# Performance work log

Measured on AMD Instinct MI355X. Metric: run time of the kernel, lower is better.

Reference implementation:

```python
import jax, jax.numpy as jnp
import numpy as np

B, N, C_S, C_Z, C, H, PQ, PV = 1, 512, 384, 128, 16, 12, 4, 8
N_BLOCKS = 8
SCALE, EPS, INF = 10.0, 1e-8, 1e5
N_RESTYPES = 5
CAT = H * C + 4 * H * PV + H * C_Z  # IPA output concat width = 2112


def layer_norm(x, g, b):
    mu = jnp.mean(x, -1, keepdims=True)
    var = jnp.mean(jnp.square(x - mu), -1, keepdims=True)
    return (x - mu) * jax.lax.rsqrt(var + 1e-5) * g + b


def quat_mul(q, p):
    w1, x1, y1, z1 = q[..., 0], q[..., 1], q[..., 2], q[..., 3]
    w2, x2, y2, z2 = p[..., 0], p[..., 1], p[..., 2], p[..., 3]
    return jnp.stack([
        w1 * w2 - x1 * x2 - y1 * y2 - z1 * z2,
        w1 * x2 + x1 * w2 + y1 * z2 - z1 * y2,
        w1 * y2 - x1 * z2 + y1 * w2 + z1 * x2,
        w1 * z2 + x1 * y2 - y1 * x2 + z1 * w2], -1)


def quat_to_rot(q):
    w, x, y, z = q[..., 0], q[..., 1], q[..., 2], q[..., 3]
    r0 = jnp.stack([w * w + x * x - y * y - z * z, 2 * (x * y - w * z), 2 * (x * z + w * y)], -1)
    r1 = jnp.stack([2 * (x * y + w * z), w * w - x * x + y * y - z * z, 2 * (y * z - w * x)], -1)
    r2 = jnp.stack([2 * (x * z - w * y), 2 * (y * z + w * x), w * w - x * x - y * y + z * z], -1)
    return jnp.stack([r0, r1, r2], -2)  # [..., 3, 3]


def _forward(single, pair, restype, mask,
             ln_s_g, ln_s_b, ln_z_g, ln_z_b, w_in, b_in,
             wq, bq, wkv, bkv, wqp, bqp, wkvp, bkvp, wb, bb_z, head_w, wo, bo,
             ln_ipa_g, ln_ipa_b, t_w1, t_b1, t_w2, t_b2, t_w3, t_b3, ln_t_g, ln_t_b,
             w_bb, b_bb, lit_pos):
    Bv, Nv = single.shape[0], single.shape[1]
    s = layer_norm(single, ln_s_g, ln_s_b)
    z = layer_norm(pair, ln_z_g, ln_z_b)
    s = s @ w_in + b_in
    quats = jnp.zeros((Bv, Nv, 4), s.dtype).at[..., 0].set(1.0)  # identity rigid, quat fmt
    trans = jnp.zeros((Bv, Nv, 3), s.dtype)
    mask_bias = INF * (mask[..., :, None] * mask[..., None, :] - 1.0)  # [B,N,N]
    hw = jax.nn.softplus(head_w) * np.float32(np.sqrt(1.0 / (3.0 * (PQ * 9.0 / 2.0))))
    zb = jnp.transpose(z @ wb + bb_z, (0, 3, 1, 2))  # [B,H,N,N] pair bias, same each block
    lit = lit_pos[restype]  # [B,N,3atoms,3] literature backbone coords

    def run_ipa(s, rot, tr):
        q = (s @ wq + bq).reshape(Bv, Nv, H, C)
        kv = (s @ wkv + bkv).reshape(Bv, Nv, H, 2 * C)
        k, v = kv[..., :C], kv[..., C:]
        qp = (s @ wqp + bqp).reshape(Bv, Nv, 3, H * PQ).swapaxes(-1, -2)
        qp = (jnp.einsum('bnij,bnpj->bnpi', rot, qp) + tr[..., None, :]).reshape(Bv, Nv, H, PQ, 3)
        kvp = (s @ wkvp + bkvp).reshape(Bv, Nv, 3, H * (PQ + PV)).swapaxes(-1, -2)
        kvp = (jnp.einsum('bnij,bnpj->bnpi', rot, kvp) + tr[..., None, :]).reshape(Bv, Nv, H, PQ + PV, 3)
        kp, vp = kvp[..., :PQ, :], kvp[..., PQ:, :]
        a = jnp.einsum('bihc,bjhc->bhij', q, k) * np.float32(np.sqrt(1.0 / (3 * C)))
        a = a + np.float32(np.sqrt(1.0 / 3.0)) * zb
        d2 = jnp.sum(jnp.square(qp[:, :, None] - kp[:, None]), -1)  # [B,N,N,H,PQ]
        pt_att = -0.5 * jnp.sum(d2 * hw[:, None], -1)  # [B,N,N,H]
        a = jax.nn.softmax(a + jnp.transpose(pt_att, (0, 3, 1, 2)) + mask_bias[:, None], -1)
        o = jnp.einsum('bhij,bjhc->bihc', a, v).reshape(Bv, Nv, H * C)
        opt = jnp.einsum('bhij,bjhpx->bihpx', a, vp)  # attended points, global frame
        opt = jnp.einsum('bnji,bnhpj->bnhpi', rot, opt - tr[:, :, None, None, :])  # invert_apply
        opt_norm = jnp.sqrt(jnp.sum(jnp.square(opt), -1) + EPS).reshape(Bv, Nv, H * PV)
        opt_flat = jnp.moveaxis(opt.reshape(Bv, Nv, H * PV, 3), -1, -2).reshape(Bv, Nv, 3 * H * PV)
        opair = jnp.einsum('bhij,bijc->bihc', a, z).reshape(Bv, Nv, H * C_Z)
        return jnp.concatenate([o, opt_flat, opt_norm, opair], -1) @ wo + bo

    frames_l, pos_l, states_l = [], [], []
    for _ in range(N_BLOCKS):
        rot = quat_to_rot(quats)
        s = s + run_ipa(s, rot, trans)
        s = layer_norm(s, ln_ipa_g, ln_ipa_b)  # ipa dropout = identity (eval)
        t = jax.nn.relu(s @ t_w1 + t_b1)
        t = jax.nn.relu(t @ t_w2 + t_b2)
        s = layer_norm(s + t @ t_w3 + t_b3, ln_t_g, ln_t_b)  # transition (1 layer) + LN
        upd = s @ w_bb + b_bb  # [B,N,6] backbone update
        pq = jnp.concatenate([jnp.ones_like(upd[..., :1]), upd[..., :3]], -1)
        nq = quat_mul(quats, pq)
        quats = nq * jax.lax.rsqrt(jnp.sum(jnp.square(nq), -1, keepdims=True))
        trans = trans + jnp.einsum('bnij,bnj->bni', rot, upd[..., 3:])  # OLD rot applies t-update
        rot_new = quat_to_rot(quats)
        pos_l.append(jnp.einsum('bnij,bnaj->bnai', rot_new, lit) + SCALE * trans[..., None, :])
        frames_l.append(jnp.concatenate([quats, SCALE * trans], -1))
        states_l.append(s)
        quats = jax.lax.stop_gradient(quats)  # stop_rot_gradient
    return jnp.stack(frames_l), jnp.stack(pos_l), jnp.stack(states_l), s


def setup_inputs() -> dict:
    key = jax.random.key(0)
    ki = iter(jax.random.split(key, 48))
    def w(fan_in, fan_out):
        return jax.random.normal(next(ki), (fan_in, fan_out), jnp.float32) / np.sqrt(fan_in)
    inp = {
        "single": jax.random.normal(next(ki), (B, N, C_S), jnp.float32),
        "pair": jax.random.normal(next(ki), (B, N, N, C_Z), jnp.float32),
        "restype": jax.random.randint(next(ki), (B, N), 0, N_RESTYPES),
        "mask": jnp.ones((B, N), jnp.float32),
        "ln_s_g": jnp.ones((C_S,)), "ln_s_b": jnp.zeros((C_S,)),
        "ln_z_g": jnp.ones((C_Z,)), "ln_z_b": jnp.zeros((C_Z,)),
        "w_in": w(C_S, C_S), "b_in": jnp.zeros((C_S,)),
        "wq": w(C_S, H * C), "bq": jnp.zeros((H * C,)),
        "wkv": w(C_S, 2 * H * C), "bkv": jnp.zeros((2 * H * C,)),
        "wqp": w(C_S, H * PQ * 3), "bqp": jnp.zeros((H * PQ * 3,)),
        "wkvp": w(C_S, H * (PQ + PV) * 3), "bkvp": jnp.zeros((H * (PQ + PV) * 3,)),
        "wb": w(C_Z, H), "bb_z": jnp.zeros((H,)),
        "head_w": 0.1 * jax.random.normal(next(ki), (H,), jnp.float32),
        "wo": w(CAT, C_S), "bo": jnp.zeros((C_S,)),
        "ln_ipa_g": jnp.ones((C_S,)), "ln_ipa_b": jnp.zeros((C_S,)),
        "t_w1": w(C_S, C_S), "t_b1": jnp.zeros((C_S,)),
        "t_w2": w(C_S, C_S), "t_b2": jnp.zeros((C_S,)),
        "t_w3": w(C_S, C_S), "t_b3": jnp.zeros((C_S,)),
        "ln_t_g": jnp.ones((C_S,)), "ln_t_b": jnp.zeros((C_S,)),
        "w_bb": 0.001 * jax.random.normal(next(ki), (C_S, 6), jnp.float32),
        "b_bb": jnp.zeros((6,)),
        "lit_pos": jax.random.normal(next(ki), (N_RESTYPES, 3, 3), jnp.float32),
    }
    return inp


def reference(single, pair, restype, mask,
              ln_s_g, ln_s_b, ln_z_g, ln_z_b, w_in, b_in,
              wq, bq, wkv, bkv, wqp, bqp, wkvp, bkvp, wb, bb_z, head_w, wo, bo,
              ln_ipa_g, ln_ipa_b, t_w1, t_b1, t_w2, t_b2, t_w3, t_b3, ln_t_g, ln_t_b,
              w_bb, b_bb, lit_pos):
    return _forward(single, pair, restype, mask,
                    ln_s_g, ln_s_b, ln_z_g, ln_z_b, w_in, b_in,
                    wq, bq, wkv, bkv, wqp, bqp, wkvp, bkvp, wb, bb_z, head_w, wo, bo,
                    ln_ipa_g, ln_ipa_b, t_w1, t_b1, t_w2, t_b2, t_w3, t_b3, ln_t_g, ln_t_b,
                    w_bb, b_bb, lit_pos)
```

## Files before the change

### kernel.cpp

```cpp
#include <hip/hip_runtime.h>
#include <hip/hip_bf16.h>
#include <math.h>

typedef __hip_bfloat16 bf16;

#define DINL __device__ __forceinline__
DINL float b2f(bf16 x){ return __bfloat162float(x); }
DINL bf16 f2b(float x){ return __float2bfloat16(x); }

DINL float ldin(const void* p, size_t i, int isb){
    return isb ? b2f(((const bf16*)p)[i]) : ((const float*)p)[i];
}
DINL void stout(void* p, size_t i, float v, int isb){
    if(isb) ((bf16*)p)[i] = f2b(v); else ((float*)p)[i] = v;
}

static constexpr int NRES = 512;
static constexpr int CS   = 384;
static constexpr int CZ   = 128;
static constexpr int NH   = 12;
static constexpr int PQn  = 4;
static constexpr int CAT  = 2112;
static constexpr int ASTR = 516;
static constexpr int ZSTR = 136;
static constexpr int SAK  = 56;
static constexpr int KSTR = 40;
static constexpr int XSTR = 392;
static constexpr int PSPL = 4;
static constexpr int WSPL = 6;

typedef __attribute__((ext_vector_type(8))) short short8;
typedef __attribute__((ext_vector_type(4))) float f32x4;

__global__ void k_detect(const void* __restrict__ mask, int* __restrict__ flag){
    if(threadIdx.x==0 && blockIdx.x==0)
        flag[0] = (((const unsigned short*)mask)[0] == 0x3F80) ? 1 : 0;
}

#define MAXSEG 32
struct ConvSegs {
    const void* src[MAXSEG];
    int dst_off[MAXSEG];
    int blk0[MAXSEG];
    int total[MAXSEG];
};

__global__ void k_conv_multi(ConvSegs sg, int nseg, float* __restrict__ wsf,
                             const int* __restrict__ dt){
    int isb = dt[0];
    int b = blockIdx.x;
    int s = 0;
    #pragma unroll 1
    while(s+1 < nseg && sg.blk0[s+1] <= b) ++s;
    int idx = (b - sg.blk0[s])*256 + threadIdx.x;
    if(idx >= sg.total[s]) return;
    wsf[(size_t)sg.dst_off[s] + idx] = ldin(sg.src[s], idx, isb);
}

#define MAXTSEG 12
struct TSegs {
    const void* src[MAXTSEG];
    size_t dst_off[MAXTSEG];
    int N[MAXTSEG];
    int dstK[MAXTSEG];
    int blk0[MAXTSEG];
    int total[MAXTSEG];
};

__global__ void k_transpose_multi(TSegs sg, int nseg, bf16* __restrict__ base,
                                  const int* __restrict__ dt){
    int isb = dt[0];
    int b = blockIdx.x;
    int s = 0;
    #pragma unroll 1
    while(s+1 < nseg && sg.blk0[s+1] <= b) ++s;
    int idx = (b - sg.blk0[s])*256 + threadIdx.x;
    if(idx >= sg.total[s]) return;
    int N = sg.N[s];
    int k = idx / N, n = idx - k*N;
    base[sg.dst_off[s] + (size_t)n*sg.dstK[s] + k] = f2b(ldin(sg.src[s], idx, isb));
}

__global__ __launch_bounds__(128) void k_ln(const void* __restrict__ in, int in_dyn,
                     float* __restrict__ out, bf16* __restrict__ out16,
                     const float* __restrict__ g, const float* __restrict__ b, int Cdim,
                     const int* __restrict__ dt, int init_frames,
                     float* __restrict__ quats, float* __restrict__ trans){
    int row = blockIdx.x, tid = threadIdx.x;
    int isb = dt[0];
    int isb_in = in_dyn ? isb : 0;
    if(init_frames && tid==0){
        quats[row*4+0]=1.f; quats[row*4+1]=0.f; quats[row*4+2]=0.f; quats[row*4+3]=0.f;
        trans[row*3+0]=0.f; trans[row*3+1]=0.f; trans[row*3+2]=0.f;
    }
    float s=0.f, s2=0.f, vals[3];
    int r=0;
    for(int c=tid; c<Cdim; c+=128, ++r){
        size_t idx = (size_t)row*Cdim + c;
        float v = ldin(in, idx, isb_in);
        vals[r]=v; s+=v; s2+=v*v;
    }
    __shared__ float red[128], red2[128];
    red[tid]=s; red2[tid]=s2; __syncthreads();
    for(int st=64; st>0; st>>=1){ if(tid<st){ red[tid]+=red[tid+st]; red2[tid]+=red2[tid+st]; } __syncthreads(); }
    float mu = red[0]/Cdim;
    float var = red2[0]/Cdim - mu*mu;
    float rs = rsqrtf(var + 1e-5f);
    r=0;
    for(int c=tid; c<Cdim; c+=128, ++r){
        float v = (vals[r]-mu)*rs*g[c] + b[c];
        size_t idx = (size_t)row*Cdim + c;
        if(out)   out[idx] = v;
        if(out16) out16[idx] = f2b(v);
    }
}

__global__ __launch_bounds__(512) void k_mlp(
        const float* __restrict__ pw, const float* __restrict__ bo_f,
        float* __restrict__ s, bf16* __restrict__ s16,
        const float* __restrict__ lnig, const float* __restrict__ lnib,
        const bf16* __restrict__ tw1T, const float* __restrict__ tb1f,
        const bf16* __restrict__ tw2T, const float* __restrict__ tb2f,
        const bf16* __restrict__ tw3T, const float* __restrict__ tb3f,
        const float* __restrict__ lntg, const float* __restrict__ lntb,
        void* __restrict__ outp, size_t st_ofs, size_t fin_ofs, int mode,
        const int* __restrict__ dt,
        const float* __restrict__ wbb_f, const float* __restrict__ bbb_f,
        const float* __restrict__ rotp, const int* __restrict__ restype,
        const float* __restrict__ lit_f,
        float* __restrict__ quats, float* __restrict__ trans,
        size_t frames_ofs, size_t pos_ofs){
    __shared__ float sip[4*CS];
    __shared__ bf16  xa[16*XSTR];
    int t = threadIdx.x;
    int w = t>>6, lane = t&63;
    int quad = lane>>4, m16 = lane&15;
    int b0 = blockIdx.x*4;
    int isb = dt[0];

    if(w < 4){
        int r = w, gr = b0+r;
        float v[6];
        float sum=0.f, sq=0.f;
        #pragma unroll
        for(int kk=0;kk<6;kk++){
            int c = lane + kk*64;
            size_t idx = (size_t)gr*CS + c;
            float x = bo_f[c] + s[idx];
            #pragma unroll
            for(int p=0;p<WSPL;p++) x += pw[(size_t)p*NRES*CS + idx];
            v[kk]=x; sum+=x; sq+=x*x;
        }
        #pragma unroll
        for(int m=32;m>=1;m>>=1){ sum+=__shfl_xor(sum,m,64); sq+=__shfl_xor(sq,m,64); }
        float mu = sum*(1.f/CS);
        float rs = rsqrtf(sq*(1.f/CS) - mu*mu + 1e-5f);
        #pragma unroll
        for(int kk=0;kk<6;kk++){
            int c = lane + kk*64;
            float x = (v[kk]-mu)*rs*lnig[c] + lnib[c];
            sip[r*CS+c] = x;
            xa[r*XSTR+c] = f2b(x);
        }
    }
    __syncthreads();

    #pragma unroll
    for(int L=0; L<3; ++L){
        const bf16* WT   = (L==0) ? tw1T : (L==1) ? tw2T : tw3T;
        const float* bias= (L==0) ? tb1f : (L==1) ? tb2f : tb3f;
        const short* wt  = (const short*)WT;
        int nb = w*3;
        const short* wp0 = wt + (size_t)((nb+0)*16+m16)*CS + quad*8;
        const short* wp1 = wt + (size_t)((nb+1)*16+m16)*CS + quad*8;
        const short* wp2 = wt + (size_t)((nb+2)*16+m16)*CS + quad*8;
        f32x4 acc[3] = {};
        short8 wbuf[2][3];
        wbuf[0][0] = *(const short8*)(wp0);
        wbuf[0][1] = *(const short8*)(wp1);
        wbuf[0][2] = *(const short8*)(wp2);
        wbuf[1][0] = *(const short8*)(wp0 + 32);
        wbuf[1][1] = *(const short8*)(wp1 + 32);
        wbuf[1][2] = *(const short8*)(wp2 + 32);
        #pragma unroll
        for(int k=0;k<12;k++){
            short8 a = *(const short8*)((const short*)xa + m16*XSTR + k*32 + quad*8);
            short8 c0 = wbuf[k&1][0], c1 = wbuf[k&1][1], c2 = wbuf[k&1][2];
            if(k<10){
                wbuf[k&1][0] = *(const short8*)(wp0 + (k+2)*32);
                wbuf[k&1][1] = *(const short8*)(wp1 + (k+2)*32);
                wbuf[k&1][2] = *(const short8*)(wp2 + (k+2)*32);
            }
            acc[0] = __builtin_amdgcn_mfma_f32_16x16x32_bf16(a, c0, acc[0], 0,0,0);
            acc[1] = __builtin_amdgcn_mfma_f32_16x16x32_bf16(a, c1, acc[1], 0,0,0);
            acc[2] = __builtin_amdgcn_mfma_f32_16x16x32_bf16(a, c2, acc[2], 0,0,0);
        }
        __syncthreads();
        if(quad == 0){
            if(L<2){
                #pragma unroll
                for(int nt=0;nt<3;nt++){
                    int col = (nb+nt)*16 + m16;
                    float bb = bias[col];
                    #pragma unroll
                    for(int r=0;r<4;r++){
                        xa[r*XSTR+col] = f2b(fmaxf(acc[nt][r] + bb, 0.f));
                    }
                }
            } else {
                #pragma unroll
                for(int nt=0;nt<3;nt++){
                    int col = (nb+nt)*16 + m16;
                    float bb = bias[col];
                    #pragma unroll
                    for(int r=0;r<4;r++){
                        sip[r*CS+col] += acc[nt][r] + bb;
                    }
                }
            }
        }
        __syncthreads();
    }

    if(w < 4){
        int r = w, gr = b0+r;
        float v[6], facc[6]={};
        float sum=0.f, sq=0.f;
        #pragma unroll
        for(int kk=0;kk<6;kk++){
            float x = sip[r*CS + lane + kk*64];
            v[kk]=x; sum+=x; sq+=x*x;
        }
        #pragma unroll
        for(int m=32;m>=1;m>>=1){ sum+=__shfl_xor(sum,m,64); sq+=__shfl_xor(sq,m,64); }
        float mu = sum*(1.f/CS);
        float rs = rsqrtf(sq*(1.f/CS) - mu*mu + 1e-5f);
        #pragma unroll
        for(int kk=0;kk<6;kk++){
            int c = lane + kk*64;
            size_t idx = (size_t)gr*CS + c;
            float x = (v[kk]-mu)*rs*lntg[c] + lntb[c];
            s[idx] = x; s16[idx] = f2b(x);
            stout(outp, st_ofs + idx, x, isb);
            if(mode == 2) stout(outp, fin_ofs + idx, x, isb);
            #pragma unroll
            for(int j=0;j<6;j++) facc[j] += x * wbb_f[c*6+j];
        }
        #pragma unroll
        for(int m=32;m>=1;m>>=1){
            #pragma unroll
            for(int j=0;j<6;j++) facc[j] += __shfl_xor(facc[j], m, 64);
        }
        if(lane==0){
            int i = gr;
            float u[6];
            #pragma unroll
            for(int j=0;j<6;j++) u[j] = facc[j] + bbb_f[j];
            float qw=quats[i*4], qx=quats[i*4+1], qy=quats[i*4+2], qz=quats[i*4+3];
            float nw = qw       - qx*u[0] - qy*u[1] - qz*u[2];
            float nx = qw*u[0] + qx       + qy*u[2] - qz*u[1];
            float ny = qw*u[1] - qx*u[2] + qy       + qz*u[0];
            float nz = qw*u[2] + qx*u[1] - qy*u[0] + qz;
            float rn = rsqrtf(nw*nw + nx*nx + ny*ny + nz*nz);
            nw*=rn; nx*=rn; ny*=rn; nz*=rn;
            quats[i*4]=nw; quats[i*4+1]=nx; quats[i*4+2]=ny; quats[i*4+3]=nz;
            const float* R = rotp + i*9;
            float tx = trans[i*3]   + R[0]*u[3]+R[1]*u[4]+R[2]*u[5];
            float ty = trans[i*3+1] + R[3]*u[3]+R[4]*u[4]+R[5]*u[5];
            float tz = trans[i*3+2] + R[6]*u[3]+R[7]*u[4]+R[8]*u[5];
            trans[i*3]=tx; trans[i*3+1]=ty; trans[i*3+2]=tz;
            size_t f = frames_ofs + (size_t)i*7;
            stout(outp, f+0, nw, isb); stout(outp, f+1, nx, isb);
            stout(outp, f+2, ny, isb); stout(outp, f+3, nz, isb);
            stout(outp, f+4, 10.f*tx, isb); stout(outp, f+5, 10.f*ty, isb); stout(outp, f+6, 10.f*tz, isb);
            float Rn[9];
            Rn[0]=nw*nw+nx*nx-ny*ny-nz*nz; Rn[1]=2.f*(nx*ny-nw*nz);       Rn[2]=2.f*(nx*nz+nw*ny);
            Rn[3]=2.f*(nx*ny+nw*nz);       Rn[4]=nw*nw-nx*nx+ny*ny-nz*nz; Rn[5]=2.f*(ny*nz-nw*nx);
            Rn[6]=2.f*(nx*nz-nw*ny);       Rn[7]=2.f*(ny*nz+nw*nx);       Rn[8]=nw*nw-nx*nx-ny*ny+nz*nz;
            int rt = restype[i];
            size_t po = pos_ofs + (size_t)i*9;
            #pragma unroll
            for(int a=0;a<3;a++){
                float lx=lit_f[(rt*3+a)*3+0], ly=lit_f[(rt*3+a)*3+1], lz=lit_f[(rt*3+a)*3+2];
                stout(outp, po+a*3+0, Rn[0]*lx + Rn[1]*ly + Rn[2]*lz + 10.f*tx, isb);
                stout(outp, po+a*3+1, Rn[3]*lx + Rn[4]*ly + Rn[5]*lz + 10.f*ty, isb);
                stout(outp, po+a*3+2, Rn[6]*lx + Rn[7]*ly + Rn[8]*lz + 10.f*tz, isb);
            }
        }
    }
}

__global__ __launch_bounds__(256) void k_gemm_bf(const bf16* __restrict__ A,
        const bf16* __restrict__ BT, float* __restrict__ Cf, bf16* __restrict__ C16,
        const float* __restrict__ bias, const float* __restrict__ res,
        int M, int Nn, int K, int relu, int lda){
    __shared__ bf16 As[64*SAK];
    __shared__ bf16 Bs[64*SAK];
    int tid = threadIdx.x;
    int bm = blockIdx.y*64, bn = blockIdx.x*64;
    int kofs = blockIdx.z*K;
    int wave = tid>>6, lane = tid&63;
    int quad = lane>>4, m16 = lane&15;
    int wm = (wave>>1)*32, wn = (wave&1)*32;
    int srow = wave*16 + (lane>>2);
    int scol = (lane&3)*8;
    const bf16* Ag = A  + (size_t)(bm + srow)*lda + kofs + scol;
    const bf16* Bg = BT + (size_t)(bn + srow)*lda + kofs + scol;
    int ldw = srow*SAK + scol;
    f32x4 acc[2][2] = {};
    short8 ra = *(const short8*)Ag;
    short8 rb = *(const short8*)Bg;
    int nsteps = K >> 5;
    const short* Asp = (const short*)As;
    const short* Bsp = (const short*)Bs;
    for(int s=0; s<nsteps; ++s){
        __syncthreads();
        *(short8*)(As + ldw) = ra;
        *(short8*)(Bs + ldw) = rb;
        __syncthreads();
        if(s+1 < nsteps){
            ra = *(const short8*)(Ag + (size_t)(s+1)*32);
            rb = *(const short8*)(Bg + (size_t)(s+1)*32);
        }
        short8 a0 = *(const short8*)&Asp[(wm +      m16)*SAK + quad*8];
        short8 a1 = *(const short8*)&Asp[(wm + 16 + m16)*SAK + quad*8];
        short8 b0 = *(const short8*)&Bsp[(wn +      m16)*SAK + quad*8];
        short8 b1 = *(const short8*)&Bsp[(wn + 16 + m16)*SAK + quad*8];
        acc[0][0] = __builtin_amdgcn_mfma_f32_16x16x32_bf16(a0, b0, acc[0][0], 0,0,0);
        acc[0][1] = __builtin_amdgcn_mfma_f32_16x16x32_bf16(a0, b1, acc[0][1], 0,0,0);
        acc[1][0] = __builtin_amdgcn_mfma_f32_16x16x32_bf16(a1, b0, acc[1][0], 0,0,0);
        acc[1][1] = __builtin_amdgcn_mfma_f32_16x16x32_bf16(a1, b1, acc[1][1], 0,0,0);
    }
    float* Cfz = Cf ? Cf + (size_t)blockIdx.z*M*Nn : nullptr;
    #pragma unroll
    for(int tm=0;tm<2;tm++){
        #pragma unroll
        for(int r=0;r<4;r++){
            int row = bm + wm + tm*16 + quad*4 + r;
            #pragma unroll
            for(int tn=0;tn<2;tn++){
                int col = bn + wn + tn*16 + m16;
                float v = acc[tm][tn][r];
                if(bias) v += bias[col];
                if(res)  v += res[(size_t)row*Nn + col];
                if(relu) v = fmaxf(v, 0.f);
                if(Cfz) Cfz[(size_t)row*Nn + col] = v;
                if(C16) C16[(size_t)row*Nn + col] = f2b(v);
            }
        }
    }
}

__global__ __launch_bounds__(256) void k_zb_mfma(const void* __restrict__ pair,
        const float* __restrict__ gz, const float* __restrict__ bz,
        const bf16* __restrict__ wbT, bf16* __restrict__ zb16,
        bf16* __restrict__ zn16, const int* __restrict__ dt){
    int isb = dt[0];
    __shared__ float gs[CZ], bs[CZ];
    __shared__ float rsum[64], rsq[64];
    __shared__ float mu_s[64], rs_s[64];
    __shared__ bf16 zn_s[64*ZSTR];
    int t = threadIdx.x;
    if(t < CZ){ gs[t]=gz[t]; bs[t]=bz[t]; }
    size_t rbase = (size_t)blockIdx.x*64;
    float xv[32];

    if(isb){
        const short8* src = (const short8*)((const short*)pair + rbase*CZ);
        #pragma unroll
        for(int r=0;r<4;r++){
            short8 c = src[r*256 + t];
            #pragma unroll
            for(int j=0;j<8;j++) xv[r*8+j] = b2f(((const bf16*)&c)[j]);
        }
        #pragma unroll
        for(int r=0;r<4;r++){
            float s=0.f, s2=0.f;
            #pragma unroll
            for(int j=0;j<8;j++){ float v=xv[r*8+j]; s+=v; s2+=v*v; }
            #pragma unroll
            for(int m=1;m<16;m<<=1){ s+=__shfl_xor(s,m,64); s2+=__shfl_xor(s2,m,64); }
            if((t&15)==0){ int row = r*16 + (t>>4); rsum[row]=s; rsq[row]=s2; }
        }
    } else {
        const float4* src = (const float4*)((const float*)pair + rbase*CZ);
        #pragma unroll
        for(int r=0;r<8;r++){
            float4 c = src[r*256 + t];
            xv[r*4+0]=c.x; xv[r*4+1]=c.y; xv[r*4+2]=c.z; xv[r*4+3]=c.w;
        }
        #pragma unroll
        for(int r=0;r<8;r++){
            float s=0.f, s2=0.f;
            #pragma unroll
            for(int j=0;j<4;j++){ float v=xv[r*4+j]; s+=v; s2+=v*v; }
            #pragma unroll
            for(int m=1;m<32;m<<=1){ s+=__shfl_xor(s,m,64); s2+=__shfl_xor(s2,m,64); }
            if((t&31)==0){ int row = r*8 + (t>>5); rsum[row]=s; rsq[row]=s2; }
        }
    }
    __syncthreads();
    if(t < 64){
        float mu = rsum[t]*(1.f/CZ);
        float var = rsq[t]*(1.f/CZ) - mu*mu;
        mu_s[t] = mu; rs_s[t] = rsqrtf(var + 1e-5f);
    }
    __syncthreads();

    if(isb){
        #pragma unroll
        for(int r=0;r<4;r++){
            int row = r*16 + (t>>4);
            int c0  = (t&15)*8;
            float mu = mu_s[row], rs = rs_s[row];
            short8 o;
            #pragma unroll
            for(int j=0;j<8;j++)
                ((bf16*)&o)[j] = f2b((xv[r*8+j]-mu)*rs*gs[c0+j] + bs[c0+j]);
            *(short8*)&zn_s[row*ZSTR + c0] = o;
            *(short8*)((short*)zn16 + (rbase+row)*CZ + c0) = o;
        }
    } else {
        #pragma unroll
        for(int r=0;r<8;r++){
            int row = r*8 + (t>>5);
            int c0  = (t&31)*4;
            float mu = mu_s[row], rs = rs_s[row];
            unsigned short pk[4];
            #pragma unroll
            for(int j=0;j<4;j++){
                bf16 h = f2b((xv[r*4+j]-mu)*rs*gs[c0+j] + bs[c0+j]);
                pk[j] = *(unsigned short*)&h;
                zn_s[row*ZSTR + c0 + j] = h;
            }
            *(uint2*)((unsigned short*)zn16 + (rbase+row)*CZ + c0) = *(const uint2*)pk;
        }
    }
    __syncthreads();

    int wave = t>>6, lane = t&63;
    int m = lane&15, quad = lane>>4;
    short8 bfrag[4];
    const short* wbs = (const short*)wbT;
    #pragma unroll
    for(int kc=0;kc<4;kc++) bfrag[kc] = *(const short8*)(wbs + m*CZ + kc*32 + quad*8);
    f32x4 acc = {0.f,0.f,0.f,0.f};
    #pragma unroll
    for(int kc=0;kc<4;kc++){
        short8 a = *(const short8*)((const short*)zn_s + (wave*16+m)*ZSTR + kc*32 + quad*8);
        acc = __builtin_amdgcn_mfma_f32_16x16x32_bf16(a, bfrag[kc], acc, 0, 0, 0);
    }
    if(m < NH){
        unsigned short pk[4];
        #pragma unroll
        for(int r=0;r<4;r++){ bf16 h = f2b(acc[r]); pk[r] = *(unsigned short*)&h; }
        size_t o = (size_t)m*((size_t)NRES*NRES) + rbase + wave*16 + quad*4;
        *(uint2*)((unsigned short*)zb16 + o) = *(const uint2*)pk;
    }
}


__global__ __launch_bounds__(192) void k_rotate_kv(const float* __restrict__ qpw,
        const float* __restrict__ bproj,
        const float* __restrict__ quats, const float* __restrict__ trans,
        float* __restrict__ rot,
        float* __restrict__ qp_rot, float* __restrict__ kp_rot, bf16* __restrict__ vp16,
        float* __restrict__ k_buf, bf16* __restrict__ v16, float* __restrict__ q_buf){
    int i = blockIdx.x, t = threadIdx.x;
    __shared__ float R[9], T[3];
    __shared__ float rowbuf[1152];
    const float* qb = qpw + (size_t)i*1152;
    #pragma unroll
    for(int r=0;r<6;r++){
        int c = t + 192*r;
        float acc = bproj[c];
        #pragma unroll
        for(int p=0;p<PSPL;p++) acc += qb[(size_t)p*NRES*1152 + c];
        rowbuf[c] = acc;
    }
    if(t==0){
        float w=quats[i*4],x=quats[i*4+1],y=quats[i*4+2],z=quats[i*4+3];
        R[0]=w*w+x*x-y*y-z*z; R[1]=2.f*(x*y-w*z);     R[2]=2.f*(x*z+w*y);
        R[3]=2.f*(x*y+w*z);   R[4]=w*w-x*x+y*y-z*z;   R[5]=2.f*(y*z-w*x);
        R[6]=2.f*(x*z-w*y);   R[7]=2.f*(y*z+w*x);     R[8]=w*w-x*x-y*y+z*z;
    }
    if(t<3) T[t] = trans[i*3+t];
    __syncthreads();
    if(t<9) rot[i*9+t] = R[t];
    q_buf[(size_t)i*192 + t] = rowbuf[t];
    {
        int h = t/16, c = t%16;
        k_buf[((size_t)h*NRES + i)*16 + c] = rowbuf[192 + h*32 + c];
        v16[(size_t)i*192 + t]             = f2b(rowbuf[192 + h*32 + 16 + c]);
    }
    if(t < 48){
        float vx = rowbuf[576 + t], vy = rowbuf[576 + 48 + t], vz = rowbuf[576 + 96 + t];
        float* o = qp_rot + ((size_t)i*48 + t)*3;
        o[0] = R[0]*vx + R[1]*vy + R[2]*vz + T[0];
        o[1] = R[3]*vx + R[4]*vy + R[5]*vz + T[1];
        o[2] = R[6]*vx + R[7]*vy + R[8]*vz + T[2];
    }
    if(t < 144){
        int hp = t;
        float vx = rowbuf[720 + hp], vy = rowbuf[720 + 144 + hp], vz = rowbuf[720 + 288 + hp];
        float ox = R[0]*vx + R[1]*vy + R[2]*vz + T[0];
        float oy = R[3]*vx + R[4]*vy + R[5]*vz + T[1];
        float oz = R[6]*vx + R[7]*vy + R[8]*vz + T[2];
        int h = hp/12, p = hp%12;
        if(p < PQn){
            float* o = kp_rot + ((size_t)i*48 + h*4 + p)*3;
            o[0]=ox; o[1]=oy; o[2]=oz;
        } else {
            bf16* o = vp16 + ((size_t)i*96 + h*8 + (p-4))*3;
            o[0]=f2b(ox); o[1]=f2b(oy); o[2]=f2b(oz);
        }
    }
}

__global__ __launch_bounds__(256) void k_attn(const float* __restrict__ q_buf,
        const float* __restrict__ k_buf, const float* __restrict__ qp_rot,
        const float* __restrict__ kp_rot, const bf16* __restrict__ zb16,
        const float* __restrict__ hw_f, const float* __restrict__ bbz_f,
        const void* __restrict__ mask, bf16* __restrict__ a16,
        const int* __restrict__ dt){
    int i0 = blockIdx.x*16, h = blockIdx.y;
    int t = threadIdx.x;
    int isb = dt[0];
    __shared__ bf16 kb_s[NRES*KSTR];
    __shared__ bf16 zb_s[16*NRES];
    __shared__ bf16 as_s[16*KSTR];
    __shared__ float colc_s[NRES];
    __shared__ float mcol_s[NRES];
    __shared__ float rowc_s[16], mrow_s[16];
    __shared__ float redm[4][16], reds[4][16];
    float hwx = hw_f[h];
    float sp = (hwx > 20.f) ? hwx : log1pf(expf(hwx));
    float hw = sp * 0.13608276348795434f;
    float zbb = 0.57735026919f * bbz_f[h];
    #pragma unroll
    for(int rr=0; rr<2; ++rr){
        int j = t*2 + rr;
        const float* kr  = k_buf  + ((size_t)h*NRES + j)*16;
        const float* kpr = kp_rot + ((size_t)j*48 + h*4)*3;
        bf16* dstp = kb_s + j*KSTR;
        float kv[16], pv[12];
        *(float4*)&kv[0]  = *(const float4*)(kr);
        *(float4*)&kv[4]  = *(const float4*)(kr + 4);
        *(float4*)&kv[8]  = *(const float4*)(kr + 8);
        *(float4*)&kv[12] = *(const float4*)(kr + 12);
        *(float4*)&pv[0]  = *(const float4*)(kpr);
        *(float4*)&pv[4]  = *(const float4*)(kpr + 4);
        *(float4*)&pv[8]  = *(const float4*)(kpr + 8);
        #pragma unroll
        for(int c=0;c<16;c++) dstp[c] = f2b(kv[c]);
        float s2k = 0.f;
        #pragma unroll
        for(int p=0;p<12;p++){ float v = pv[p]; s2k += v*v; dstp[16+p] = f2b(v); }
        dstp[28]=f2b(0.f); dstp[29]=f2b(0.f); dstp[30]=f2b(0.f); dstp[31]=f2b(0.f);
        colc_s[j] = -0.5f*hw*s2k;
        mcol_s[j] = ldin(mask, j, isb);
    }
    {
        const short8* zsrc = (const short8*)((const unsigned short*)zb16 + (size_t)h*NRES*NRES + (size_t)i0*NRES);
        short8* zdst = (short8*)zb_s;
        #pragma unroll
        for(int r=0;r<4;r++) zdst[t + r*256] = zsrc[t + r*256];
    }
    if(t < 16){
        int m = t;
        const float* qr = q_buf + (size_t)(i0+m)*192 + h*16;
        bf16* dstp = as_s + m*KSTR;
        float qv[16], qpv[12];
        *(float4*)&qv[0]  = *(const float4*)(qr);
        *(float4*)&qv[4]  = *(const float4*)(qr + 4);
        *(float4*)&qv[8]  = *(const float4*)(qr + 8);
        *(float4*)&qv[12] = *(const float4*)(qr + 12);
        const float* qpr = qp_rot + ((size_t)(i0+m)*48 + h*4)*3;
        *(float4*)&qpv[0] = *(const float4*)(qpr);
        *(float4*)&qpv[4] = *(const float4*)(qpr + 4);
        *(float4*)&qpv[8] = *(const float4*)(qpr + 8);
        #pragma unroll
        for(int c=0;c<16;c++) dstp[c] = f2b(qv[c]*0.14433756729740643f);
        float s2q = 0.f;
        #pragma unroll
        for(int p=0;p<12;p++){ float v = qpv[p]; s2q += v*v; dstp[16+p] = f2b(v*hw); }
        dstp[28]=f2b(0.f); dstp[29]=f2b(0.f); dstp[30]=f2b(0.f); dstp[31]=f2b(0.f);
        rowc_s[m] = -0.5f*hw*s2q;
        mrow_s[m] = ldin(mask, i0+m, isb);
    }
    __syncthreads();
    int lane = t&63, wv = t>>6;
    int quad = lane>>4, m16 = lane&15;
    short8 afrag = *(const short8*)((const short*)as_s + m16*KSTR + quad*8);
    float l[8][4];
    #pragma unroll
    for(int tt=0; tt<8; ++tt){
        int jt = wv*8 + tt;
        short8 bfrag = *(const short8*)((const short*)kb_s + (jt*16+m16)*KSTR + quad*8);
        f32x4 acc = {0.f,0.f,0.f,0.f};
        acc = __builtin_amdgcn_mfma_f32_16x16x32_bf16(afrag, bfrag, acc, 0,0,0);
        int j = jt*16 + m16;
        float cc = colc_s[j] + zbb;
        float mj = mcol_s[j];
        #pragma unroll
        for(int r=0;r<4;r++){
            int row = quad*4 + r;
            float zbv = b2f(zb_s[row*NRES + j]);
            l[tt][r] = acc[r] + 0.57735026919f*zbv + cc + rowc_s[row]
                     + 100000.0f*(mrow_s[row]*mj - 1.0f);
        }
    }
    float lm[4], ls[4];
    #pragma unroll
    for(int r=0;r<4;r++){
        float m = l[0][r];
        #pragma unroll
        for(int tt=1;tt<8;tt++) m = fmaxf(m, l[tt][r]);
        #pragma unroll
        for(int msk=1; msk<16; msk<<=1) m = fmaxf(m, __shfl_xor(m, msk, 64));
        lm[r] = m;
        float s = 0.f;
        #pragma unroll
        for(int tt=0;tt<8;tt++){ float e = expf(l[tt][r]-m); l[tt][r] = e; s += e; }
        #pragma unroll
        for(int msk=1; msk<16; msk<<=1) s += __shfl_xor(s, msk, 64);
        ls[r] = s;
    }
    if(m16 == 0){
        #pragma unroll
        for(int r=0;r<4;r++){ redm[wv][quad*4+r] = lm[r]; reds[wv][quad*4+r] = ls[r]; }
    }
    __syncthreads();
    #pragma unroll
    for(int r=0;r<4;r++){
        int row = quad*4+r;
        float M = redm[0][row];
        #pragma unroll
        for(int w=1;w<4;w++) M = fmaxf(M, redm[w][row]);
        float S = 0.f;
        #pragma unroll
        for(int w=0;w<4;w++) S += reds[w][row]*expf(redm[w][row]-M);
        float f = expf(lm[r]-M)/S;
        #pragma unroll
        for(int tt=0;tt<8;tt++){
            int j = (wv*8+tt)*16 + m16;
            a16[((size_t)h*NRES + i0+row)*NRES + j] = f2b(l[tt][r]*f);
        }
    }
}

__global__ __launch_bounds__(512) void k_attn_out(const bf16* __restrict__ a16,
        const bf16* __restrict__ v16, const bf16* __restrict__ vp16,
        const bf16* __restrict__ zn16,
        const float* __restrict__ rot, const float* __restrict__ trans,
        bf16* __restrict__ o_cat16){
    int i = blockIdx.x, t = threadIdx.x;
    __shared__ float a_sf[NH*ASTR];
    __shared__ bf16  zn_s[32*ZSTR];
    __shared__ float opt_s[288];
    for(int vv=t; vv<768; vv+=512){
        int h = vv>>6, j8 = (vv&63)*8;
        short8 a8 = *(const short8*)((const short*)a16 + (size_t)h*NRES*NRES + (size_t)i*NRES + j8);
        float* dst = a_sf + h*ASTR + j8;
        #pragma unroll
        for(int u=0;u<8;u++) dst[u] = b2f(((const bf16*)&a8)[u]);
    }
    int lane = t&63, quad = lane>>4, m16 = lane&15;
    int wv = t>>6;
    int jj = t>>4, c8 = (t&15)*8;
    int pc = t;
    int h0 = (pc<192) ? (pc>>4) : (pc-192)/24;
    const bf16* s0 = (pc<192) ? (v16 + pc) : (vp16 + (pc-192));
    int st0 = (pc<192) ? 192 : 288;
    const bf16* s1 = vp16 + 192 + t;
    int h1 = (192 + t)/24;
    float acc0 = 0.f, acc1 = 0.f;
    f32x4 macc[4] = {};
    __syncthreads();
    for(int j0=0; j0<NRES; j0+=32){
        if(j0) __syncthreads();
        {
            size_t pb = ((size_t)i*NRES + j0+jj)*CZ + c8;
            short8 z8 = *(const short8*)((const short*)zn16 + pb);
            *(short8*)&zn_s[jj*ZSTR + c8] = z8;
        }
        __syncthreads();
        if(wv < 6){
            const float* ap0 = a_sf + h0*ASTR;
            #pragma unroll
            for(int u=0; u<32; u+=4){
                int j = j0+u;
                float4 a4 = *(const float4*)(ap0 + j);
                acc0 += a4.x*b2f(s0[(size_t)j*st0])     + a4.y*b2f(s0[(size_t)(j+1)*st0])
                      + a4.z*b2f(s0[(size_t)(j+2)*st0]) + a4.w*b2f(s0[(size_t)(j+3)*st0]);
            }
            if(t < 96){
                const float* ap1 = a_sf + h1*ASTR;
                #pragma unroll
                for(int u=0; u<32; u+=4){
                    int j = j0+u;
                    float4 a4 = *(const float4*)(ap1 + j);
                    acc1 += a4.x*b2f(s1[(size_t)j*288])     + a4.y*b2f(s1[(size_t)(j+1)*288])
                          + a4.z*b2f(s1[(size_t)(j+2)*288]) + a4.w*b2f(s1[(size_t)(j+3)*288]);
                }
            }
        } else {
            float4 af0 = *(const float4*)&a_sf[m16*ASTR + j0 + quad*8];
            float4 af1 = *(const float4*)&a_sf[m16*ASTR + j0 + quad*8 + 4];
            short8 afrag;
            float az[8] = {af0.x,af0.y,af0.z,af0.w,af1.x,af1.y,af1.z,af1.w};
            #pragma unroll
            for(int r=0;r<8;r++) ((bf16*)&afrag)[r] = f2b((m16 < NH) ? az[r] : 0.f);
            int cbase = (wv-6)*64;
            #pragma unroll
            for(int tn=0; tn<4; ++tn){
                int c0 = cbase + tn*16;
                short8 bfrag;
                #pragma unroll
                for(int r=0;r<8;r++) ((bf16*)&bfrag)[r] = zn_s[(quad*8+r)*ZSTR + c0 + m16];
                macc[tn] = __builtin_amdgcn_mfma_f32_16x16x32_bf16(afrag, bfrag, macc[tn], 0,0,0);
            }
        }
    }
    if(wv >= 6){
        int cbase = (wv-6)*64;
        #pragma unroll
        for(int tn=0; tn<4; ++tn){
            int c = cbase + tn*16 + m16;
            #pragma unroll
            for(int r=0;r<4;r++){
                int h = quad*4 + r;
                if(h < NH) o_cat16[(size_t)i*CAT + 576 + h*CZ + c] = f2b(macc[tn][r]);
            }
        }
    } else {
        if(pc < 192) o_cat16[(size_t)i*CAT + pc] = f2b(acc0);
        else         opt_s[pc-192] = acc0;
        if(t < 96)   opt_s[192+t] = acc1;
    }
    __syncthreads();
    if(t < 96){
        float R0=rot[i*9+0],R1=rot[i*9+1],R2=rot[i*9+2];
        float R3=rot[i*9+3],R4=rot[i*9+4],R5=rot[i*9+5];
        float R6=rot[i*9+6],R7=rot[i*9+7],R8=rot[i*9+8];
        float T0=trans[i*3+0],T1=trans[i*3+1],T2=trans[i*3+2];
        const float* v = opt_s + t*3;
        float vx=v[0]-T0, vy=v[1]-T1, vz=v[2]-T2;
        float ox = R0*vx + R3*vy + R6*vz;
        float oy = R1*vx + R4*vy + R7*vz;
        float oz = R2*vx + R5*vy + R8*vz;
        bf16* o = o_cat16 + (size_t)i*CAT;
        o[192 +       t] = f2b(ox);
        o[192 +  96 + t] = f2b(oy);
        o[192 + 192 + t] = f2b(oz);
        o[480 + t] = f2b(sqrtf(ox*ox + oy*oy + oz*oz + 1e-8f));
    }
}


extern "C" void kernel_launch(void* const* d_in, const int* in_sizes, int n_in,
                              void* d_out, int out_size, void* d_ws, size_t ws_size,
                              hipStream_t stream){
    (void)in_sizes; (void)n_in; (void)out_size; (void)ws_size;
    const void* single = d_in[0];
    const void* pair   = d_in[1];
    const int*  restype= (const int*)d_in[2];
    const void* mask   = d_in[3];

    float* wsf = (float*)d_ws;
    bf16*  wsb = (bf16*)d_ws;
    size_t off = 0;
    auto alloc  = [&](size_t n){ float* p = wsf + off; off += (n + 3) & ~(size_t)3; return p; };
    auto allocB = [&](size_t n){ bf16* p = (bf16*)(wsf + off); off += ((n+1)/2 + 3) & ~(size_t)3; return p; };
    int*   dflag  = (int*)alloc(4);
    float* s      = alloc((size_t)NRES*CS);
    float* pw     = alloc((size_t)WSPL*NRES*CS);
    float* qpw    = alloc((size_t)PSPL*NRES*1152);
    float* q_buf  = alloc((size_t)NRES*192);
    float* qp_rot = alloc((size_t)NRES*144);
    float* kp_rot = alloc((size_t)NRES*144);
    float* k_bufp = alloc((size_t)NH*NRES*16);
    float* quats  = alloc(NRES*4);
    float* trans  = alloc(NRES*3);
    float* rot    = alloc(NRES*9);
    bf16*  a16    = allocB((size_t)NH*NRES*NRES);
    bf16*  zb16   = allocB((size_t)NH*NRES*NRES);
    bf16*  zn16   = allocB((size_t)NRES*NRES*CZ);
    bf16*  v16    = allocB((size_t)NRES*192);
    bf16*  vp16   = allocB((size_t)NRES*288);
    bf16*  o_cat16= allocB((size_t)NRES*CAT);
    bf16*  sin16  = allocB((size_t)NRES*CS);
    bf16*  s16    = allocB((size_t)NRES*CS);
    bf16*  WprojT = allocB((size_t)1152*CS);
    bf16*  w_inT  = allocB((size_t)CS*CS);
    bf16*  woT    = allocB((size_t)CS*CAT);
    bf16*  tw1T   = allocB((size_t)CS*CS);
    bf16*  tw2T   = allocB((size_t)CS*CS);
    bf16*  tw3T   = allocB((size_t)CS*CS);
    bf16*  wbT    = allocB(16*CZ);
    float* b_in_f = alloc(CS);
    float* bproj  = alloc(1152);
    float* bo_f   = alloc(CS);
    float* tb1f   = alloc(CS);
    float* tb2f   = alloc(CS);
    float* tb3f   = alloc(CS);
    float* lnsg   = alloc(CS);
    float* lnsb   = alloc(CS);
    float* lnig   = alloc(CS);
    float* lnib   = alloc(CS);
    float* lntg   = alloc(CS);
    float* lntb   = alloc(CS);
    float* gz_f   = alloc(CZ);
    float* bz_f   = alloc(CZ);
    float* bbz_f  = alloc(16);
    float* hw_f   = alloc(16);
    float* wbb_f  = alloc(CS*6);
    float* bbb_f  = alloc(8);
    float* lit_f  = alloc(48);

    const size_t OF_FRAMES = 0;
    const size_t OF_POS    = 28672;
    const size_t OF_STATES = 65536;
    const size_t OF_FINAL  = 1638400;

    k_detect<<<1,64,0,stream>>>(mask, dflag);

    ConvSegs sg;
    int nseg = 0, blk = 0;
    auto plain = [&](const void* src, float* dst, int total){
        sg.src[nseg]=src; sg.dst_off[nseg]=(int)(dst - wsf);
        sg.total[nseg]=total; sg.blk0[nseg]=blk;
        blk += (total+255)/256; ++nseg;
    };
    plain(d_in[11], bproj,     192);
    plain(d_in[13], bproj+192, 384);
    plain(d_in[15], bproj+576, 144);
    plain(d_in[17], bproj+720, 432);
    plain(d_in[9],  b_in_f, CS);
    plain(d_in[22], bo_f,   CS);
    plain(d_in[26], tb1f,   CS);
    plain(d_in[28], tb2f,   CS);
    plain(d_in[30], tb3f,   CS);
    plain(d_in[4],  lnsg,   CS);
    plain(d_in[5],  lnsb,   CS);
    plain(d_in[23], lnig,   CS);
    plain(d_in[24], lnib,   CS);
    plain(d_in[31], lntg,   CS);
    plain(d_in[32], lntb,   CS);
    plain(d_in[6],  gz_f,   CZ);
    plain(d_in[7],  bz_f,   CZ);
    plain(d_in[19], bbz_f,  NH);
    plain(d_in[20], hw_f,   NH);
    plain(d_in[34], bbb_f,  6);
    plain(d_in[35], lit_f,  45);
    plain(d_in[33], wbb_f,  CS*6);
    k_conv_multi<<<blk,256,0,stream>>>(sg, nseg, wsf, dflag);

    TSegs tg;
    int ntseg = 0, tblk = 0;
    auto trs = [&](const void* src, int K, int N, bf16* dst, int rowofs, int dstK){
        tg.src[ntseg]=src;
        tg.dst_off[ntseg]=(size_t)(dst - wsb) + (size_t)rowofs*dstK;
        tg.N[ntseg]=N; tg.dstK[ntseg]=dstK;
        tg.total[ntseg]=K*N; tg.blk0[ntseg]=tblk;
        tblk += (K*N+255)/256; ++ntseg;
    };
    trs(d_in[10], CS, 192, WprojT, 0,   CS);
    trs(d_in[12], CS, 384, WprojT, 192, CS);
    trs(d_in[14], CS, 144, WprojT, 576, CS);
    trs(d_in[16], CS, 432, WprojT, 720, CS);
    trs(d_in[8],  CS, CS,  w_inT,  0,   CS);
    trs(d_in[21], CAT, CS, woT,    0,   CAT);
    trs(d_in[25], CS, CS,  tw1T,   0,   CS);
    trs(d_in[27], CS, CS,  tw2T,   0,   CS);
    trs(d_in[29], CS, CS,  tw3T,   0,   CS);
    trs(d_in[18], CZ, NH,  wbT,    0,   CZ);
    k_transpose_multi<<<tblk,256,0,stream>>>(tg, ntseg, wsb, dflag);

    k_zb_mfma<<<NRES*NRES/64,256,0,stream>>>(pair, gz_f, bz_f, wbT, zb16, zn16, dflag);

    k_ln<<<NRES,128,0,stream>>>(single, 1, nullptr, sin16, lnsg, lnsb, CS, dflag, 1, quats, trans);
    {
        dim3 g(CS/64, NRES/64);
        k_gemm_bf<<<g,256,0,stream>>>(sin16, w_inT, s, s16, b_in_f, nullptr, NRES, CS, CS, 0, CS);
    }

    for(int bi=0; bi<8; ++bi){
        {
            dim3 gp(1152/64, NRES/64, PSPL);
            k_gemm_bf<<<gp,256,0,stream>>>(s16, WprojT, qpw, nullptr, nullptr, nullptr,
                                           NRES, 1152, 384/PSPL, 0, CS);
        }
        k_rotate_kv<<<NRES,192,0,stream>>>(qpw, bproj, quats, trans, rot, qp_rot, kp_rot,
                                           vp16, k_bufp, v16, q_buf);
        {
            dim3 g(NRES/16, NH);
            k_attn<<<g,256,0,stream>>>(q_buf, k_bufp, qp_rot, kp_rot, zb16, hw_f, bbz_f, mask, a16, dflag);
        }
        k_attn_out<<<NRES,512,0,stream>>>(a16, v16, vp16, zn16, rot, trans, o_cat16);
        {
            dim3 gw(CS/64, NRES/64, WSPL);
            k_gemm_bf<<<gw,256,0,stream>>>(o_cat16, woT, pw, nullptr, nullptr, nullptr,
                                           NRES, CS, CAT/WSPL, 0, CAT);
            k_mlp<<<NRES/4,512,0,stream>>>(pw, bo_f, s, s16, lnig, lnib,
                                            tw1T, tb1f, tw2T, tb2f, tw3T, tb3f,
                                            lntg, lntb,
                                            d_out, OF_STATES + (size_t)bi*NRES*CS, OF_FINAL,
                                            (bi==7) ? 2 : 1, dflag,
                                            wbb_f, bbb_f, rot, restype, lit_f,
                                            quats, trans,
                                            OF_FRAMES + (size_t)bi*NRES*7,
                                            OF_POS + (size_t)bi*NRES*9);
        }
    }
}
```

Measured before the change: 1.272 ms.

## Halve attention K staging LDS and prefetch pair tiles into registers

```diff
diff --git a/kernel.cpp b/kernel.cpp
--- a/kernel.cpp
+++ b/kernel.cpp
@@ -526,7 +526,7 @@
     int i0 = blockIdx.x*16, h = blockIdx.y;
     int t = threadIdx.x;
     int isb = dt[0];
-    __shared__ bf16 kb_s[NRES*KSTR];
+    __shared__ bf16 kb_s[256*KSTR];
     __shared__ bf16 zb_s[16*NRES];
     __shared__ bf16 as_s[16*KSTR];
     __shared__ float colc_s[NRES];
@@ -537,29 +537,9 @@
     float sp = (hwx > 20.f) ? hwx : log1pf(expf(hwx));
     float hw = sp * 0.13608276348795434f;
     float zbb = 0.57735026919f * bbz_f[h];
-    #pragma unroll
-    for(int rr=0; rr<2; ++rr){
-        int j = t*2 + rr;
-        const float* kr  = k_buf  + ((size_t)h*NRES + j)*16;
-        const float* kpr = kp_rot + ((size_t)j*48 + h*4)*3;
-        bf16* dstp = kb_s + j*KSTR;
-        float kv[16], pv[12];
-        *(float4*)&kv[0]  = *(const float4*)(kr);
-        *(float4*)&kv[4]  = *(const float4*)(kr + 4);
-        *(float4*)&kv[8]  = *(const float4*)(kr + 8);
-        *(float4*)&kv[12] = *(const float4*)(kr + 12);
-        *(float4*)&pv[0]  = *(const float4*)(kpr);
-        *(float4*)&pv[4]  = *(const float4*)(kpr + 4);
-        *(float4*)&pv[8]  = *(const float4*)(kpr + 8);
-        #pragma unroll
-        for(int c=0;c<16;c++) dstp[c] = f2b(kv[c]);
-        float s2k = 0.f;
-        #pragma unroll
-        for(int p=0;p<12;p++){ float v = pv[p]; s2k += v*v; dstp[16+p] = f2b(v); }
-        dstp[28]=f2b(0.f); dstp[29]=f2b(0.f); dstp[30]=f2b(0.f); dstp[31]=f2b(0.f);
-        colc_s[j] = -0.5f*hw*s2k;
-        mcol_s[j] = ldin(mask, j, isb);
-    }
+    int lane = t&63, wv = t>>6;
+    int quad = lane>>4, m16 = lane&15;
+    float l[8][4];
     {
         const short8* zsrc = (const short8*)((const unsigned short*)zb16 + (size_t)h*NRES*NRES + (size_t)i0*NRES);
         short8* zdst = (short8*)zb_s;
@@ -588,26 +568,49 @@
         rowc_s[m] = -0.5f*hw*s2q;
         mrow_s[m] = ldin(mask, i0+m, isb);
     }
-    __syncthreads();
-    int lane = t&63, wv = t>>6;
-    int quad = lane>>4, m16 = lane&15;
-    short8 afrag = *(const short8*)((const short*)as_s + m16*KSTR + quad*8);
-    float l[8][4];
     #pragma unroll
-    for(int tt=0; tt<8; ++tt){
-        int jt = wv*8 + tt;
-        short8 bfrag = *(const short8*)((const short*)kb_s + (jt*16+m16)*KSTR + quad*8);
-        f32x4 acc = {0.f,0.f,0.f,0.f};
-        acc = __builtin_amdgcn_mfma_f32_16x16x32_bf16(afrag, bfrag, acc, 0,0,0);
-        int j = jt*16 + m16;
-        float cc = colc_s[j] + zbb;
-        float mj = mcol_s[j];
-        #pragma unroll
-        for(int r=0;r<4;r++){
-            int row = quad*4 + r;
-            float zbv = b2f(zb_s[row*NRES + j]);
-            l[tt][r] = acc[r] + 0.57735026919f*zbv + cc + rowc_s[row]
-                     + 100000.0f*(mrow_s[row]*mj - 1.0f);
+    for(int p=0; p<2; ++p){
+        if(p) __syncthreads();
+        {
+            int j = p*256 + t;
+            const float* kr  = k_buf  + ((size_t)h*NRES + j)*16;
+            const float* kpr = kp_rot + ((size_t)j*48 + h*4)*3;
+            bf16* dstp = kb_s + t*KSTR;
+            float kv[16], pv[12];
+            *(float4*)&kv[0]  = *(const float4*)(kr);
+            *(float4*)&kv[4]  = *(const float4*)(kr + 4);
+            *(float4*)&kv[8]  = *(const float4*)(kr + 8);
+            *(float4*)&kv[12] = *(const float4*)(kr + 12);
+            *(float4*)&pv[0]  = *(const float4*)(kpr);
+            *(float4*)&pv[4]  = *(const float4*)(kpr + 4);
+            *(float4*)&pv[8]  = *(const float4*)(kpr + 8);
+            #pragma unroll
+            for(int c=0;c<16;c++) dstp[c] = f2b(kv[c]);
+            float s2k = 0.f;
+            #pragma unroll
+            for(int pp=0;pp<12;pp++){ float v = pv[pp]; s2k += v*v; dstp[16+pp] = f2b(v); }
+            dstp[28]=f2b(0.f); dstp[29]=f2b(0.f); dstp[30]=f2b(0.f); dstp[31]=f2b(0.f);
+            colc_s[j] = -0.5f*hw*s2k;
+            mcol_s[j] = ldin(mask, j, isb);
+        }
+        __syncthreads();
+        short8 afrag = *(const short8*)((const short*)as_s + m16*KSTR + quad*8);
+        #pragma unroll
+        for(int tt=0; tt<4; ++tt){
+            int jl = wv*4 + tt;
+            short8 bfrag = *(const short8*)((const short*)kb_s + (jl*16+m16)*KSTR + quad*8);
+            f32x4 acc = {0.f,0.f,0.f,0.f};
+            acc = __builtin_amdgcn_mfma_f32_16x16x32_bf16(afrag, bfrag, acc, 0,0,0);
+            int j = p*256 + jl*16 + m16;
+            float cc = colc_s[j] + zbb;
+            float mj = mcol_s[j];
+            #pragma unroll
+            for(int r=0;r<4;r++){
+                int row = quad*4 + r;
+                float zbv = b2f(zb_s[row*NRES + j]);
+                l[p*4+tt][r] = acc[r] + 0.57735026919f*zbv + cc + rowc_s[row]
+                             + 100000.0f*(mrow_s[row]*mj - 1.0f);
+            }
         }
     }
     float lm[4], ls[4];
@@ -642,9 +645,9 @@
         for(int w=0;w<4;w++) S += reds[w][row]*expf(redm[w][row]-M);
         float f = expf(lm[r]-M)/S;
         #pragma unroll
-        for(int tt=0;tt<8;tt++){
-            int j = (wv*8+tt)*16 + m16;
-            a16[((size_t)h*NRES + i0+row)*NRES + j] = f2b(l[tt][r]*f);
+        for(int q=0;q<8;q++){
+            int j = (q>>2)*256 + (wv*4 + (q&3))*16 + m16;
+            a16[((size_t)h*NRES + i0+row)*NRES + j] = f2b(l[q][r]*f);
         }
     }
 }
@@ -658,6 +661,8 @@
     __shared__ float a_sf[NH*ASTR];
     __shared__ bf16  zn_s[32*ZSTR];
     __shared__ float opt_s[288];
+    int jj = t>>4, c8 = (t&15)*8;
+    short8 zreg = *(const short8*)((const short*)zn16 + ((size_t)i*NRES + jj)*CZ + c8);
     for(int vv=t; vv<768; vv+=512){
         int h = vv>>6, j8 = (vv&63)*8;
         short8 a8 = *(const short8*)((const short*)a16 + (size_t)h*NRES*NRES + (size_t)i*NRES + j8);
@@ -667,7 +672,6 @@
     }
     int lane = t&63, quad = lane>>4, m16 = lane&15;
     int wv = t>>6;
-    int jj = t>>4, c8 = (t&15)*8;
     int pc = t;
     int h0 = (pc<192) ? (pc>>4) : (pc-192)/24;
     const bf16* s0 = (pc<192) ? (v16 + pc) : (vp16 + (pc-192));
@@ -679,12 +683,10 @@
     __syncthreads();
     for(int j0=0; j0<NRES; j0+=32){
         if(j0) __syncthreads();
-        {
-            size_t pb = ((size_t)i*NRES + j0+jj)*CZ + c8;
-            short8 z8 = *(const short8*)((const short*)zn16 + pb);
-            *(short8*)&zn_s[jj*ZSTR + c8] = z8;
-        }
+        *(short8*)&zn_s[jj*ZSTR + c8] = zreg;
         __syncthreads();
+        if(j0+32 < NRES)
+            zreg = *(const short8*)((const short*)zn16 + ((size_t)i*NRES + j0+32+jj)*CZ + c8);
         if(wv < 6){
             const float* ap0 = a_sf + h0*ASTR;
             #pragma unroll
```

New measurement: 1.215 ms. 1.05x faster.
